# Kernel optimization log

Hardware: AMD Instinct MI355X
Metric: run time of the kernel (lower is better)

Reference implementation:

```python
import jax, jax.numpy as jnp
import numpy as np
from jax import lax

B, L = 8, 128
V, P = 30000, 50
EMB, POS = 300, 30
H = 256            # rnn_hidden per direction
H2 = 2 * H         # BiLSTM output dim
NBIO, NLAB = 9, 10
ROUNDS = 2
IN = EMB + POS
NEG = -100000000000.0


def setup_inputs() -> dict:
    key = jax.random.key(0)
    ks = jax.random.split(key, 25)
    tokens = jax.random.randint(ks[0], (B, L), 1, V)
    pos = jax.random.randint(ks[1], (B, L), 1, P)
    lens = jax.random.randint(ks[2], (B,), L // 2, L + 1)
    mask_s = (jnp.arange(L)[None, :] < lens[:, None]).astype(jnp.float32)

    def g(k, shape, s=0.05):
        return jax.random.normal(k, shape, dtype=jnp.float32) * s

    return dict(
        tokens=tokens, pos=pos, mask_s=mask_s,
        emb=g(ks[3], (V, EMB), 0.5), pos_emb=g(ks[4], (P, POS), 0.5),
        Wih_f=g(ks[5], (4 * H, IN)), Whh_f=g(ks[6], (4 * H, H)), b_f=g(ks[7], (4 * H,)),
        Wih_b=g(ks[8], (4 * H, IN)), Whh_b=g(ks[9], (4 * H, H)), b_b=g(ks[10], (4 * H,)),
        Wg_ih=g(ks[11], (3 * H2, NBIO)), Wg_hh=g(ks[12], (3 * H2, H2)),
        bg_ih=g(ks[13], (3 * H2,)), bg_hh=g(ks[14], (3 * H2,)),
        Wr_ih=g(ks[15], (3 * H2, NLAB)), Wr_hh=g(ks[16], (3 * H2, H2)),
        br_ih=g(ks[17], (3 * H2,)), br_hh=g(ks[18], (3 * H2,)),
        W_Lr=g(ks[19], (H2, 2 * H2)), b_Lr=g(ks[20], (H2,)),
        W_Cr=g(ks[21], (NLAB, H2)), b_Cr=g(ks[22], (NLAB,)),
        W_Cg=g(ks[23], (NBIO, H2)), b_Cg=g(ks[24], (NBIO,)),
    )


def lstm_dir(x, m, Wih, Whh, b, reverse):
    # x: [B,L,IN], m: [B,L]. Masked updates emulate pack_padded_sequence
    # (state held at padded steps; padded outputs zeroed by caller).
    Bn = x.shape[0]
    h0 = jnp.zeros((Bn, H), x.dtype)
    c0 = jnp.zeros((Bn, H), x.dtype)

    def step(carry, inp):
        h, c = carry
        xt, mt = inp  # [B,IN], [B,1]
        gates = xt @ Wih.T + h @ Whh.T + b
        i, f, g, o = jnp.split(gates, 4, axis=-1)
        i = jax.nn.sigmoid(i); f = jax.nn.sigmoid(f)
        g = jnp.tanh(g); o = jax.nn.sigmoid(o)
        c_new = f * c + i * g
        h_new = o * jnp.tanh(c_new)
        h = mt * h_new + (1.0 - mt) * h
        c = mt * c_new + (1.0 - mt) * c
        return (h, c), h

    xs = (jnp.swapaxes(x, 0, 1), m.T[:, :, None])
    _, hs = lax.scan(step, (h0, c0), xs, reverse=reverse)
    return jnp.swapaxes(hs, 0, 1)  # [B,L,H]


def gru_cell(x, h, Wih, Whh, bih, bhh):
    gi = x @ Wih.T + bih
    gh = h @ Whh.T + bhh
    ir, iz, inn = jnp.split(gi, 3, axis=-1)
    hr, hz, hn = jnp.split(gh, 3, axis=-1)
    r = jax.nn.sigmoid(ir + hr)
    z = jax.nn.sigmoid(iz + hz)
    n = jnp.tanh(inn + r * hn)
    return (1.0 - z) * n + z * h


def pair_scores(Hr, W_Lr, b_Lr, W_Cr, b_Cr):
    # Lr([e1;e2]) split: e12 @ W_Lr.T = e1 @ W1.T + e2 @ W2.T (avoids 4H concat)
    W1, W2 = W_Lr[:, :H2], W_Lr[:, H2:]
    a = jnp.einsum('blh,oh->blo', Hr, W1)  # [B,L,H2]
    b2 = jnp.einsum('blh,oh->blo', Hr, W2)
    e = jax.nn.relu(a[:, :, None, :] + b2[:, None, :, :] + b_Lr)  # [B,L,L,H2]
    return jax.nn.sigmoid(jnp.einsum('bsth,kh->bstk', e, W_Cr) + b_Cr)  # [B,L,L,NLAB]


def reference(tokens, pos, mask_s, emb, pos_emb,
              Wih_f, Whh_f, b_f, Wih_b, Whh_b, b_b,
              Wg_ih, Wg_hh, bg_ih, bg_hh,
              Wr_ih, Wr_hh, br_ih, br_hh,
              W_Lr, b_Lr, W_Cr, b_Cr, W_Cg, b_Cg):
    x = jnp.concatenate([emb[tokens], pos_emb[pos]], axis=2)  # [B,L,IN]
    hf = lstm_dir(x, mask_s, Wih_f, Whh_f, b_f, reverse=False)
    hb = lstm_dir(x, mask_s, Wih_b, Whh_b, b_b, reverse=True)
    Henc = jnp.concatenate([hf, hb], axis=2) * mask_s[:, :, None]  # [B,L,H2]

    m2 = mask_s[:, :, None] * mask_s[:, None, :]  # [B,L,L] pair mask
    m3 = m2[:, :, :, None]                        # [B,L,L,1]

    Hc, Hg, Hr = Henc, Henc, Henc
    for _ in range(ROUNDS):
        prob_Cg = jax.nn.softmax(Hg @ W_Cg.T + b_Cg, axis=2)        # [B,L,NBIO]
        prob_Cr = pair_scores(Hr, W_Lr, b_Lr, W_Cr, b_Cr)            # [B,L,L,NLAB]
        prob_Cr = jnp.where(m3 > 0, prob_Cr, NEG)
        prob_Cr = prob_Cr.max(axis=2)                                # [B,L,NLAB]
        hflat = Hc.reshape(-1, H2)
        Hg = gru_cell(prob_Cg.reshape(-1, NBIO), hflat, Wg_ih, Wg_hh, bg_ih, bg_hh).reshape(Hc.shape)
        Hr = gru_cell(prob_Cr.reshape(-1, NLAB), hflat, Wr_ih, Wr_hh, br_ih, br_hh).reshape(Hc.shape)
        Hc = Hc + Hr + Hg

    logits_Cg = jax.nn.log_softmax(Hg @ W_Cg.T + b_Cg, axis=2) * mask_s[:, :, None]
    logits_Cr = pair_scores(Hr, W_Lr, b_Lr, W_Cr, b_Cr) * m3
    return logits_Cg, logits_Cr
```

## Files before the change

### kernel.cpp

```cpp
#include <hip/hip_runtime.h>
#include <hip/hip_bf16.h>
#include <stdint.h>

#define DEVI __device__ __forceinline__

static constexpr int Bn = 8, Ln = 128;
static constexpr int EMBc = 300, POSc = 30, INc = 330;
static constexpr int KPAD = 384;
static constexpr int Hc = 256, H2c = 512, G4 = 1024, G3 = 1536;
static constexpr int G2 = 2048;
static constexpr int GHW = 3072;
static constexpr int NBIOc = 9, NLABc = 10;
static constexpr float NEGc = -100000000000.0f;

typedef __attribute__((ext_vector_type(8))) short bf16x8;
typedef __attribute__((ext_vector_type(4))) float f32x4;

DEVI float sigf(float x) { return 1.0f / (1.0f + __expf(-x)); }

DEVI unsigned short b16rne(float f) {
    union { float f; unsigned u; } v; v.f = f;
    unsigned u = v.u;
    return (unsigned short)((u + 0x7FFFu + ((u >> 16) & 1u)) >> 16);
}

__global__ void k_prep0(const int* __restrict__ tok, const int* __restrict__ pos,
                        const float* __restrict__ emb, const float* __restrict__ pemb,
                        const float* __restrict__ WihF, const float* __restrict__ WihB,
                        const float* __restrict__ bF, const float* __restrict__ bB,
                        ushort* __restrict__ x, ushort* __restrict__ WihFB,
                        float* __restrict__ biasFB) {
    int i = blockIdx.x * 256 + threadIdx.x;
    const int N0 = Bn * Ln * KPAD;
    const int N1 = N0 + G2 * KPAD;
    if (i < N0) {
        int bl = i / KPAD, c = i - bl * KPAD;
        float v = 0.f;
        if (c < EMBc) v = emb[tok[bl] * EMBc + c];
        else if (c < INc) v = pemb[pos[bl] * POSc + (c - EMBc)];
        x[i] = b16rne(v);
    } else if (i < N1) {
        int w = i - N0;
        int r = w / KPAD, c = w - r * KPAD;
        float v = 0.f;
        if (c < INc) v = (r < G4) ? WihF[(size_t)r * INc + c] : WihB[(size_t)(r - G4) * INc + c];
        WihFB[w] = b16rne(v);
    } else if (i < N1 + G2) {
        int j = i - N1;
        biasFB[j] = (j < G4) ? bF[j] : bB[j - G4];
    }
}

DEVI void gemm_tile(const ushort* __restrict__ A, const ushort* __restrict__ B,
                    const float* __restrict__ bias, float* __restrict__ C,
                    int N, int K, int m0, int n0,
                    ushort (*As)[72], ushort (*Bs)[72]) {
    int tid = threadIdx.x;
    int lane = tid & 63, wv = tid >> 6;
    int mw = (wv >> 1) * 32, nw = (wv & 1) * 32;
    int lr16 = lane & 15, g4 = lane >> 4;
    f32x4 acc[2][2] = {};
    for (int k0 = 0; k0 < K; k0 += 64) {
#pragma unroll
        for (int it = 0; it < 2; it++) {
            int idx = tid + it * 256;
            int r = idx >> 3, ch = idx & 7;
            uint4 av = *(const uint4*)(A + (size_t)(m0 + r) * K + k0 + ch * 8);
            *(uint4*)(&As[r][ch * 8]) = av;
            uint4 bv2 = *(const uint4*)(B + (size_t)(n0 + r) * K + k0 + ch * 8);
            *(uint4*)(&Bs[r][ch * 8]) = bv2;
        }
        __syncthreads();
#pragma unroll
        for (int ks = 0; ks < 2; ks++) {
            bf16x8 af[2], bfr[2];
#pragma unroll
            for (int i = 0; i < 2; i++) {
                af[i]  = *(const bf16x8*)(&As[mw + i * 16 + lr16][ks * 32 + g4 * 8]);
                bfr[i] = *(const bf16x8*)(&Bs[nw + i * 16 + lr16][ks * 32 + g4 * 8]);
            }
#pragma unroll
            for (int i = 0; i < 2; i++)
#pragma unroll
                for (int j = 0; j < 2; j++)
                    acc[i][j] = __builtin_amdgcn_mfma_f32_16x16x32_bf16(af[i], bfr[j], acc[i][j], 0, 0, 0);
        }
        __syncthreads();
    }
#pragma unroll
    for (int i = 0; i < 2; i++)
#pragma unroll
        for (int j = 0; j < 2; j++)
#pragma unroll
            for (int r2 = 0; r2 < 4; r2++) {
                int mm = m0 + mw + i * 16 + g4 * 4 + r2;
                int nn = n0 + nw + j * 16 + lr16;
                C[(size_t)mm * N + nn] = acc[i][j][r2] + (bias ? bias[nn] : 0.f);
            }
}

__global__ __launch_bounds__(256) void k_xproj(
    const ushort* __restrict__ x_bf, const ushort* __restrict__ WihFB,
    const float* __restrict__ biasFB, float* __restrict__ Xpre,
    const float* __restrict__ Wg_hh, const float* __restrict__ Wr_hh,
    const float* __restrict__ W_Lr, const float* __restrict__ bg_hh,
    const float* __restrict__ br_hh,
    ushort* __restrict__ WhhGR, ushort* __restrict__ WLrAB, float* __restrict__ biasGR) {
    int bid = blockIdx.x;
    __shared__ __align__(16) ushort As[64][72];
    __shared__ __align__(16) ushort Bs[64][72];
    if (bid < 512) {
        int nt = bid & 31, mt = bid >> 5;
        gemm_tile(x_bf, WihFB, biasFB, Xpre, G2, KPAD, mt * 64, nt * 64, As, Bs);
        return;
    }
    const int stride = 128 * 256;
    int pid = (bid - 512) * 256 + threadIdx.x;
    for (int idx = pid; idx < GHW * H2c; idx += stride) {
        int r = idx >> 9, c = idx & 511;
        float v = (r < G3) ? Wg_hh[(size_t)r * H2c + c] : Wr_hh[(size_t)(r - G3) * H2c + c];
        WhhGR[idx] = b16rne(v);
    }
    for (int idx = pid; idx < G4 * H2c; idx += stride) {
        int r = idx >> 9, c = idx & 511;
        float v = (r < H2c) ? W_Lr[(size_t)r * (2 * H2c) + c]
                            : W_Lr[(size_t)(r - H2c) * (2 * H2c) + H2c + c];
        WLrAB[idx] = b16rne(v);
    }
    for (int idx = pid; idx < GHW; idx += stride)
        biasGR[idx] = (idx < G3) ? bg_hh[idx] : br_hh[idx - G3];
}

__global__ __launch_bounds__(512) void k_lstm_mfma(
    const float* __restrict__ Xpre, const float* __restrict__ WhhF,
    const float* __restrict__ WhhB, const float* __restrict__ mask,
    float* __restrict__ Henc, ushort* __restrict__ HencB,
    unsigned long long* __restrict__ hG) {
    const int blk = blockIdx.x;
    const int d = blk >> 2, q = blk & 3;
    const float* Whh = d ? WhhB : WhhF;
    const int tid = threadIdx.x;
    const int lane = tid & 63, wv = tid >> 6;
    const int lr16 = lane & 15, g4 = lane >> 4;

    __shared__ __align__(16) uint32_t hlds[2][8 * 136];
    __shared__ float Glds[256][9];

    bf16x8 aw[16];
#pragma unroll
    for (int jt2 = 0; jt2 < 2; jt2++) {
        int jt = wv * 2 + jt2;
        int lr = jt * 16 + lr16;
        int g = lr >> 6, jj = lr & 63;
        int R = g * 256 + q * 64 + jj;
        const float* wr = Whh + (size_t)R * 256;
#pragma unroll
        for (int kt = 0; kt < 8; kt++) {
            int k0 = kt * 32 + g4 * 8;
            float4 f0 = *(const float4*)(wr + k0);
            float4 f1 = *(const float4*)(wr + k0 + 4);
            bf16x8 a;
            a[0] = (short)b16rne(f0.x); a[1] = (short)b16rne(f0.y);
            a[2] = (short)b16rne(f0.z); a[3] = (short)b16rne(f0.w);
            a[4] = (short)b16rne(f1.x); a[5] = (short)b16rne(f1.y);
            a[6] = (short)b16rne(f1.z); a[7] = (short)b16rne(f1.w);
            aw[jt2 * 8 + kt] = a;
        }
    }

    const int jj_t = tid & 63, b_t = tid >> 6;
    float hval = 0.f, cval = 0.f;
    const int bcol = lane & 15;
    const int bb = lane & 7;
    const int u1 = tid + 512;

    for (int s = 0; s < Ln; s++) {
        const int t = d ? (Ln - 1 - s) : s;

        const float* xrow = Xpre + ((size_t)(b_t * Ln + t)) * G2 + d * G4 + q * 64 + jj_t;
        float xg0 = xrow[0], xg1 = xrow[256], xg2 = xrow[512], xg3 = xrow[768];
        float mval = mask[b_t * Ln + t];

        const unsigned long long* slot = hG + ((size_t)(s & 1) * 2 + d) * 1024;
        unsigned long long ea, eb;
        do {
            ea = __hip_atomic_load(slot + tid, __ATOMIC_RELAXED, __HIP_MEMORY_SCOPE_AGENT);
            eb = __hip_atomic_load(slot + u1,  __ATOMIC_RELAXED, __HIP_MEMORY_SCOPE_AGENT);
        } while ((unsigned)(ea >> 32) != (unsigned)s || (unsigned)(eb >> 32) != (unsigned)s);
        uint32_t* hb = hlds[s & 1];
        hb[(tid >> 7) * 136 + (tid & 127)] = (uint32_t)ea;
        hb[(u1 >> 7) * 136 + (u1 & 127)]  = (uint32_t)eb;
        __syncthreads();

        bf16x8 bv[8];
#pragma unroll
        for (int kt = 0; kt < 8; kt++)
            bv[kt] = *(const bf16x8*)(&hb[bb * 136 + kt * 16 + g4 * 4]);

        f32x4 acc0 = {0.f, 0.f, 0.f, 0.f}, acc1 = {0.f, 0.f, 0.f, 0.f};
#pragma unroll
        for (int kt = 0; kt < 8; kt++) {
            acc0 = __builtin_amdgcn_mfma_f32_16x16x32_bf16(aw[kt], bv[kt], acc0, 0, 0, 0);
            acc1 = __builtin_amdgcn_mfma_f32_16x16x32_bf16(aw[8 + kt], bv[kt], acc1, 0, 0, 0);
        }

        if (bcol < 8) {
            int lrb0 = (wv * 2 + 0) * 16 + g4 * 4;
            int lrb1 = (wv * 2 + 1) * 16 + g4 * 4;
#pragma unroll
            for (int r2 = 0; r2 < 4; r2++) Glds[lrb0 + r2][bcol] = acc0[r2];
#pragma unroll
            for (int r2 = 0; r2 < 4; r2++) Glds[lrb1 + r2][bcol] = acc1[r2];
        }
        __syncthreads();

        float iv = sigf(xg0 + Glds[jj_t][b_t]);
        float fv = sigf(xg1 + Glds[64 + jj_t][b_t]);
        float gv = tanhf(xg2 + Glds[128 + jj_t][b_t]);
        float ov = sigf(xg3 + Glds[192 + jj_t][b_t]);
        float cn = fv * cval + iv * gv;
        float hn = ov * tanhf(cn);
        float hv = mval * hn + (1.f - mval) * hval;
        cval = mval * cn + (1.f - mval) * cval;
        hval = hv;

        int hbits = (int)b16rne(hv);
        int pbits = __shfl_xor(hbits, 1);
        if ((jj_t & 1) == 0) {
            uint32_t dataw = ((uint32_t)hbits & 0xFFFFu) | ((uint32_t)pbits << 16);
            unsigned long long word = ((unsigned long long)(unsigned)(s + 1) << 32) | dataw;
            __hip_atomic_store(hG + ((size_t)((s + 1) & 1) * 2 + d) * 1024 +
                                   b_t * 128 + q * 32 + (jj_t >> 1),
                               word, __ATOMIC_RELAXED, __HIP_MEMORY_SCOPE_AGENT);
        }
        float ho = hv * mval;
        size_t hidx = ((size_t)(b_t * Ln + t)) * H2c + d * Hc + q * 64 + jj_t;
        Henc[hidx] = ho;
        HencB[hidx] = b16rne(ho);
        __syncthreads();
    }
}

__global__ __launch_bounds__(256) void k_mega(
    int nGh,
    const ushort* __restrict__ Agh, const ushort* __restrict__ Bgh,
    const float* __restrict__ biasGh, float* __restrict__ Cgh,
    const ushort* __restrict__ Apc, const ushort* __restrict__ Bpc,
    float* __restrict__ Cpc,
    const float* __restrict__ Hp9, const float* __restrict__ W9,
    const float* __restrict__ b9, float* __restrict__ out9) {
    int bid = blockIdx.x;
    __shared__ __align__(16) ushort As[64][72];
    __shared__ __align__(16) ushort Bs[64][72];
    if (bid < nGh) {
        int nt = bid % 48, mt = bid / 48;
        gemm_tile(Agh, Bgh, biasGh, Cgh, GHW, H2c, mt * 64, nt * 64, As, Bs);
    } else if (bid < nGh + 256) {
        int b2 = bid - nGh;
        int nt = b2 & 15, mt = b2 >> 4;
        gemm_tile(Apc, Bpc, nullptr, Cpc, G4, H2c, mt * 64, nt * 64, As, Bs);
    } else {
        int b3 = bid - nGh - 256;
        int lane = threadIdx.x & 63, wvv = threadIdx.x >> 6;
        int row = b3 * 4 + wvv;
        const float4* h4 = (const float4*)(Hp9 + (size_t)row * H2c + lane * 8);
        float4 h0 = h4[0], h1 = h4[1];
        float acc[NBIOc];
#pragma unroll
        for (int k = 0; k < NBIOc; k++) {
            const float4* w4 = (const float4*)(W9 + (size_t)k * H2c + lane * 8);
            float4 w0 = w4[0], w1 = w4[1];
            acc[k] = h0.x * w0.x + h0.y * w0.y + h0.z * w0.z + h0.w * w0.w +
                     h1.x * w1.x + h1.y * w1.y + h1.z * w1.z + h1.w * w1.w;
        }
#pragma unroll
        for (int off = 32; off >= 1; off >>= 1)
#pragma unroll
            for (int k = 0; k < NBIOc; k++) acc[k] += __shfl_down(acc[k], off);
        if (lane == 0) {
#pragma unroll
            for (int k = 0; k < NBIOc; k++) out9[(size_t)row * NBIOc + k] = acc[k] + b9[k];
        }
    }
}

__global__ __launch_bounds__(128) void k_pairgru(
    const float* __restrict__ Cp, const float* __restrict__ bL,
    const float* __restrict__ WCr, const float* __restrict__ bCr,
    const float* __restrict__ mask, const float* __restrict__ cg,
    const float* __restrict__ gh,
    const float* __restrict__ Wg_ih, const float* __restrict__ bg_ih,
    const float* __restrict__ Wr_ih, const float* __restrict__ br_ih,
    const float* __restrict__ hprev,
    float* __restrict__ Hg_out, float* __restrict__ Hcb_out,
    ushort* __restrict__ Hrb_out, ushort* __restrict__ Hcbb_out) {
    int m = blockIdx.x;
    int b = m >> 7;
    __shared__ __align__(16) float As[H2c];
    __shared__ __align__(16) float Ws[NLABc][H2c];
    __shared__ float red[NLABc][128];
    __shared__ float pCr_s[NLABc];
    int tid = threadIdx.x;
    for (int i = tid; i < H2c; i += 128) As[i] = Cp[(size_t)m * G4 + i] + bL[i];
    for (int i = tid; i < NLABc * H2c; i += 128) Ws[i / H2c][i % H2c] = WCr[i];
    __syncthreads();
    {
        int t = tid;
        float m3 = mask[m] * mask[b * Ln + t];
        float outv[NLABc];
        if (m3 > 0.f) {
            float4 acc[NLABc];
#pragma unroll
            for (int k = 0; k < NLABc; k++) acc[k] = make_float4(0.f, 0.f, 0.f, 0.f);
            const float4* B4 = (const float4*)(Cp + (size_t)(b * Ln + t) * G4 + H2c);
            const float4* A4 = (const float4*)As;
            for (int qq = 0; qq < H2c / 4; qq++) {
                float4 a = A4[qq], bb = B4[qq];
                float4 e;
                e.x = fmaxf(a.x + bb.x, 0.f);
                e.y = fmaxf(a.y + bb.y, 0.f);
                e.z = fmaxf(a.z + bb.z, 0.f);
                e.w = fmaxf(a.w + bb.w, 0.f);
#pragma unroll
                for (int k = 0; k < NLABc; k++) {
                    float4 w = *(const float4*)(&Ws[k][qq * 4]);
                    acc[k].x += e.x * w.x; acc[k].y += e.y * w.y;
                    acc[k].z += e.z * w.z; acc[k].w += e.w * w.w;
                }
            }
#pragma unroll
            for (int k = 0; k < NLABc; k++)
                outv[k] = sigf(acc[k].x + acc[k].y + acc[k].z + acc[k].w + bCr[k]);
        } else {
#pragma unroll
            for (int k = 0; k < NLABc; k++) outv[k] = NEGc;
        }
#pragma unroll
        for (int k = 0; k < NLABc; k++) red[k][tid] = outv[k];
    }
    __syncthreads();
    for (int off = 64; off >= 1; off >>= 1) {
        if (tid < off) {
#pragma unroll
            for (int k = 0; k < NLABc; k++) red[k][tid] = fmaxf(red[k][tid], red[k][tid + off]);
        }
        __syncthreads();
    }
    if (tid < NLABc) pCr_s[tid] = red[tid][0];
    __syncthreads();

    float v[NBIOc], mx = -3.4e38f;
#pragma unroll
    for (int k = 0; k < NBIOc; k++) { v[k] = cg[m * NBIOc + k]; mx = fmaxf(mx, v[k]); }
    float ssum = 0.f;
#pragma unroll
    for (int k = 0; k < NBIOc; k++) { v[k] = __expf(v[k] - mx); ssum += v[k]; }
    float inv = 1.f / ssum;
#pragma unroll
    for (int k = 0; k < NBIOc; k++) v[k] *= inv;

    const float* g1b = gh + (size_t)m * GHW;
#pragma unroll
    for (int u = 0; u < 4; u++) {
        int j = tid + u * 128;
        size_t i = (size_t)m * H2c + j;

        float gr = bg_ih[j], gz = bg_ih[H2c + j], gn = bg_ih[2 * H2c + j];
#pragma unroll
        for (int k = 0; k < NBIOc; k++) {
            float pv = v[k];
            gr += Wg_ih[(size_t)j * NBIOc + k] * pv;
            gz += Wg_ih[(size_t)(H2c + j) * NBIOc + k] * pv;
            gn += Wg_ih[(size_t)(2 * H2c + j) * NBIOc + k] * pv;
        }
        float hp = hprev[i];
        float r1 = sigf(gr + g1b[j]);
        float z1 = sigf(gz + g1b[H2c + j]);
        float n1 = tanhf(gn + r1 * g1b[2 * H2c + j]);
        float hg = (1.f - z1) * n1 + z1 * hp;

        float rr = br_ih[j], rz = br_ih[H2c + j], rn = br_ih[2 * H2c + j];
#pragma unroll
        for (int k = 0; k < NLABc; k++) {
            float pv = pCr_s[k];
            rr += Wr_ih[(size_t)j * NLABc + k] * pv;
            rz += Wr_ih[(size_t)(H2c + j) * NLABc + k] * pv;
            rn += Wr_ih[(size_t)(2 * H2c + j) * NLABc + k] * pv;
        }
        const float* g2b = g1b + G3;
        float r2 = sigf(rr + g2b[j]);
        float z2 = sigf(rz + g2b[H2c + j]);
        float n2 = tanhf(rn + r2 * g2b[2 * H2c + j]);
        float hr = (1.f - z2) * n2 + z2 * hp;

        float hc = hp + hr + hg;
        Hg_out[i] = hg;
        Hcb_out[i] = hc;
        Hrb_out[i] = b16rne(hr);
        Hcbb_out[i] = b16rne(hc);
    }
}

__global__ __launch_bounds__(128) void k_final_out(
    const float* __restrict__ Cp, const float* __restrict__ bL,
    const float* __restrict__ WCr, const float* __restrict__ bCr,
    const float* __restrict__ mask, const float* __restrict__ cg,
    float* __restrict__ outp) {
    int bid = blockIdx.x;
    int tid = threadIdx.x;
    if (bid >= Bn * Ln) {
        int r = (bid - Bn * Ln) * 128 + tid;
        float v[NBIOc], mx = -3.4e38f;
#pragma unroll
        for (int k = 0; k < NBIOc; k++) { v[k] = cg[r * NBIOc + k]; mx = fmaxf(mx, v[k]); }
        float s = 0.f;
#pragma unroll
        for (int k = 0; k < NBIOc; k++) s += __expf(v[k] - mx);
        float lse = mx + __logf(s);
        float m = mask[r];
#pragma unroll
        for (int k = 0; k < NBIOc; k++) outp[r * NBIOc + k] = (v[k] - lse) * m;
        return;
    }
    int bs = bid;
    int b = bs >> 7;
    __shared__ __align__(16) float As[H2c];
    __shared__ __align__(16) float Ws[NLABc][H2c];
    for (int i = tid; i < H2c; i += 128) As[i] = Cp[(size_t)bs * G4 + i] + bL[i];
    for (int i = tid; i < NLABc * H2c; i += 128) Ws[i / H2c][i % H2c] = WCr[i];
    __syncthreads();
    int t = tid;
    float m3 = mask[bs] * mask[b * Ln + t];
    float outv[NLABc];
    if (m3 > 0.f) {
        float4 acc[NLABc];
#pragma unroll
        for (int k = 0; k < NLABc; k++) acc[k] = make_float4(0.f, 0.f, 0.f, 0.f);
        const float4* B4 = (const float4*)(Cp + (size_t)(b * Ln + t) * G4 + H2c);
        const float4* A4 = (const float4*)As;
        for (int qq = 0; qq < H2c / 4; qq++) {
            float4 a = A4[qq], bb = B4[qq];
            float4 e;
            e.x = fmaxf(a.x + bb.x, 0.f);
            e.y = fmaxf(a.y + bb.y, 0.f);
            e.z = fmaxf(a.z + bb.z, 0.f);
            e.w = fmaxf(a.w + bb.w, 0.f);
#pragma unroll
            for (int k = 0; k < NLABc; k++) {
                float4 w = *(const float4*)(&Ws[k][qq * 4]);
                acc[k].x += e.x * w.x; acc[k].y += e.y * w.y;
                acc[k].z += e.z * w.z; acc[k].w += e.w * w.w;
            }
        }
#pragma unroll
        for (int k = 0; k < NLABc; k++)
            outv[k] = sigf(acc[k].x + acc[k].y + acc[k].z + acc[k].w + bCr[k]);
    } else {
#pragma unroll
        for (int k = 0; k < NLABc; k++) outv[k] = 0.f;
    }
    size_t base = (size_t)(Bn * Ln * NBIOc) + ((size_t)bs * Ln + t) * NLABc;
#pragma unroll
    for (int k = 0; k < NLABc; k++) outp[base + k] = outv[k];
}

extern "C" void kernel_launch(void* const* d_in, const int* in_sizes, int n_in,
                              void* d_out, int out_size, void* d_ws, size_t ws_size,
                              hipStream_t stream) {
    const int*   tok   = (const int*)d_in[0];
    const int*   pos   = (const int*)d_in[1];
    const float* mask  = (const float*)d_in[2];
    const float* emb   = (const float*)d_in[3];
    const float* pemb  = (const float*)d_in[4];
    const float* WihF  = (const float*)d_in[5];
    const float* WhhF  = (const float*)d_in[6];
    const float* bF    = (const float*)d_in[7];
    const float* WihB  = (const float*)d_in[8];
    const float* WhhB  = (const float*)d_in[9];
    const float* bB    = (const float*)d_in[10];
    const float* Wg_ih = (const float*)d_in[11];
    const float* Wg_hh = (const float*)d_in[12];
    const float* bg_ih = (const float*)d_in[13];
    const float* bg_hh = (const float*)d_in[14];
    const float* Wr_ih = (const float*)d_in[15];
    const float* Wr_hh = (const float*)d_in[16];
    const float* br_ih = (const float*)d_in[17];
    const float* br_hh = (const float*)d_in[18];
    const float* W_Lr  = (const float*)d_in[19];
    const float* b_Lr  = (const float*)d_in[20];
    const float* W_Cr  = (const float*)d_in[21];
    const float* b_Cr  = (const float*)d_in[22];
    const float* W_Cg  = (const float*)d_in[23];
    const float* b_Cg  = (const float*)d_in[24];

    float* outp = (float*)d_out;
    float* ws = (float*)d_ws;

    unsigned long long* hG = (unsigned long long*)ws;
    size_t off = 8192;
    auto alloc = [&](size_t n) { off = (off + 3) & ~(size_t)3; float* p = ws + off; off += n; return p; };
    auto allocU = [&](size_t n_us) { off = (off + 3) & ~(size_t)3; ushort* p = (ushort*)(ws + off); off += (n_us + 1) / 2; return p; };

    float* R1 = alloc((size_t)G4 * GHW);
    float* Xpre = R1;
    float* gh   = R1;
    ushort* WihFB_bf = (ushort*)(R1 + (size_t)G4 * G2);
    ushort* x_bf     = (ushort*)(R1 + (size_t)G4 * G2 + 393216);
    float*  biasFB   = R1 + (size_t)G4 * G2 + 393216 + 196608;

    float*  pairC    = alloc((size_t)G4 * G4);
    ushort* WhhGR_bf = allocU((size_t)GHW * H2c);
    ushort* WLrAB_bf = allocU((size_t)G4 * H2c);
    float*  biasGR   = alloc(GHW);
    float*  Henc     = alloc((size_t)Bn * Ln * H2c);
    ushort* Henc_bf  = allocU((size_t)Bn * Ln * H2c);
    float*  Hg       = alloc((size_t)Bn * Ln * H2c);
    float*  Hcb      = alloc((size_t)Bn * Ln * H2c);
    ushort* Hr_bf    = allocU((size_t)Bn * Ln * H2c);
    ushort* Hcb_bf   = allocU((size_t)Bn * Ln * H2c);
    float*  cg       = alloc((size_t)Bn * Ln * NBIOc);
    (void)ws_size; (void)in_sizes; (void)n_in; (void)out_size;

    hipMemsetAsync(hG, 0, 8192 * sizeof(float), stream);

    {
        int total = Bn * Ln * KPAD + G2 * KPAD + G2;
        k_prep0<<<(total + 255) / 256, 256, 0, stream>>>(
            tok, pos, emb, pemb, WihF, WihB, bF, bB, x_bf, WihFB_bf, biasFB);
    }

    k_xproj<<<640, 256, 0, stream>>>(x_bf, WihFB_bf, biasFB, Xpre,
                                     Wg_hh, Wr_hh, W_Lr, bg_hh, br_hh,
                                     WhhGR_bf, WLrAB_bf, biasGR);

    k_lstm_mfma<<<8, 512, 0, stream>>>(Xpre, WhhF, WhhB, mask, Henc, Henc_bf, hG);

    const float*  Hgs    = Henc;
    const ushort* Hrs_bf = Henc_bf;
    const float*  Hcs    = Henc;
    const ushort* Hcs_bf = Henc_bf;
    for (int r = 0; r < 2; r++) {
        k_mega<<<768 + 512, 256, 0, stream>>>(768,
            Hcs_bf, WhhGR_bf, biasGR, gh,
            Hrs_bf, WLrAB_bf, pairC,
            Hgs, W_Cg, b_Cg, cg);
        k_pairgru<<<Bn * Ln, 128, 0, stream>>>(
            pairC, b_Lr, W_Cr, b_Cr, mask, cg, gh,
            Wg_ih, bg_ih, Wr_ih, br_ih, Hcs,
            Hg, Hcb, Hr_bf, Hcb_bf);
        Hgs = Hg; Hrs_bf = Hr_bf; Hcs = Hcb; Hcs_bf = Hcb_bf;
    }

    k_mega<<<512, 256, 0, stream>>>(0,
        nullptr, nullptr, nullptr, nullptr,
        Hrs_bf, WLrAB_bf, pairC,
        Hgs, W_Cg, b_Cg, cg);
    k_final_out<<<Bn * Ln + 8, 128, 0, stream>>>(pairC, b_Lr, W_Cr, b_Cr, mask, cg, outp);
}
```

Baseline: 432.5 us.

## Fold hG memset into prep kernel, transpose GRU input weights, move LSTM barrier

The hG flag buffer is now zeroed inside k_prep0 instead of by a separate hipMemsetAsync, which removes one launch. The small GRU input-weight matrices are transposed once in k_xproj so k_pairgru reads them coalesced across j rather than with a stride of 9 or 10. In the LSTM loop the barrier is moved before the Henc stores, so those global writes can overlap with the next step's work. These are three small, unrelated tweaks, and their combined effect on total time is likely minor.

Measured after the change: 432.9 us. About the same (+0.1%).

```diff
diff --git a/kernel.cpp b/kernel.cpp
--- a/kernel.cpp
+++ b/kernel.cpp
@@ -29,10 +29,12 @@
                         const float* __restrict__ WihF, const float* __restrict__ WihB,
                         const float* __restrict__ bF, const float* __restrict__ bB,
                         ushort* __restrict__ x, ushort* __restrict__ WihFB,
-                        float* __restrict__ biasFB) {
+                        float* __restrict__ biasFB, uint32_t* __restrict__ hG32) {
     int i = blockIdx.x * 256 + threadIdx.x;
     const int N0 = Bn * Ln * KPAD;
     const int N1 = N0 + G2 * KPAD;
+    const int N2 = N1 + G2;
+    const int N3 = N2 + 8192;
     if (i < N0) {
         int bl = i / KPAD, c = i - bl * KPAD;
         float v = 0.f;
@@ -45,9 +47,11 @@
         float v = 0.f;
         if (c < INc) v = (r < G4) ? WihF[(size_t)r * INc + c] : WihB[(size_t)(r - G4) * INc + c];
         WihFB[w] = b16rne(v);
-    } else if (i < N1 + G2) {
+    } else if (i < N2) {
         int j = i - N1;
         biasFB[j] = (j < G4) ? bF[j] : bB[j - G4];
+    } else if (i < N3) {
+        __hip_atomic_store(&hG32[i - N2], 0u, __ATOMIC_RELAXED, __HIP_MEMORY_SCOPE_AGENT);
     }
 }
 
@@ -105,7 +109,9 @@
     const float* __restrict__ Wg_hh, const float* __restrict__ Wr_hh,
     const float* __restrict__ W_Lr, const float* __restrict__ bg_hh,
     const float* __restrict__ br_hh,
-    ushort* __restrict__ WhhGR, ushort* __restrict__ WLrAB, float* __restrict__ biasGR) {
+    const float* __restrict__ Wg_ih, const float* __restrict__ Wr_ih,
+    ushort* __restrict__ WhhGR, ushort* __restrict__ WLrAB, float* __restrict__ biasGR,
+    float* __restrict__ WgihT, float* __restrict__ WrihT) {
     int bid = blockIdx.x;
     __shared__ __align__(16) ushort As[64][72];
     __shared__ __align__(16) ushort Bs[64][72];
@@ -129,6 +135,14 @@
     }
     for (int idx = pid; idx < GHW; idx += stride)
         biasGR[idx] = (idx < G3) ? bg_hh[idx] : br_hh[idx - G3];
+    for (int idx = pid; idx < NBIOc * G3; idx += stride) {
+        int k = idx / G3, rj = idx - k * G3;
+        WgihT[idx] = Wg_ih[(size_t)rj * NBIOc + k];
+    }
+    for (int idx = pid; idx < NLABc * G3; idx += stride) {
+        int k = idx / G3, rj = idx - k * G3;
+        WrihT[idx] = Wr_ih[(size_t)rj * NLABc + k];
+    }
 }
 
 __global__ __launch_bounds__(512) void k_lstm_mfma(
@@ -233,11 +247,12 @@
                                    b_t * 128 + q * 32 + (jj_t >> 1),
                                word, __ATOMIC_RELAXED, __HIP_MEMORY_SCOPE_AGENT);
         }
+        __syncthreads();
+
         float ho = hv * mval;
         size_t hidx = ((size_t)(b_t * Ln + t)) * H2c + d * Hc + q * 64 + jj_t;
         Henc[hidx] = ho;
         HencB[hidx] = b16rne(ho);
-        __syncthreads();
     }
 }
 
@@ -289,8 +304,8 @@
     const float* __restrict__ WCr, const float* __restrict__ bCr,
     const float* __restrict__ mask, const float* __restrict__ cg,
     const float* __restrict__ gh,
-    const float* __restrict__ Wg_ih, const float* __restrict__ bg_ih,
-    const float* __restrict__ Wr_ih, const float* __restrict__ br_ih,
+    const float* __restrict__ WgihT, const float* __restrict__ bg_ih,
+    const float* __restrict__ WrihT, const float* __restrict__ br_ih,
     const float* __restrict__ hprev,
     float* __restrict__ Hg_out, float* __restrict__ Hcb_out,
     ushort* __restrict__ Hrb_out, ushort* __restrict__ Hcbb_out) {
@@ -369,9 +384,9 @@
 #pragma unroll
         for (int k = 0; k < NBIOc; k++) {
             float pv = v[k];
-            gr += Wg_ih[(size_t)j * NBIOc + k] * pv;
-            gz += Wg_ih[(size_t)(H2c + j) * NBIOc + k] * pv;
-            gn += Wg_ih[(size_t)(2 * H2c + j) * NBIOc + k] * pv;
+            gr += WgihT[k * G3 + j] * pv;
+            gz += WgihT[k * G3 + H2c + j] * pv;
+            gn += WgihT[k * G3 + 2 * H2c + j] * pv;
         }
         float hp = hprev[i];
         float r1 = sigf(gr + g1b[j]);
@@ -383,9 +398,9 @@
 #pragma unroll
         for (int k = 0; k < NLABc; k++) {
             float pv = pCr_s[k];
-            rr += Wr_ih[(size_t)j * NLABc + k] * pv;
-            rz += Wr_ih[(size_t)(H2c + j) * NLABc + k] * pv;
-            rn += Wr_ih[(size_t)(2 * H2c + j) * NLABc + k] * pv;
+            rr += WrihT[k * G3 + j] * pv;
+            rz += WrihT[k * G3 + H2c + j] * pv;
+            rn += WrihT[k * G3 + 2 * H2c + j] * pv;
         }
         const float* g2b = g1b + G3;
         float r2 = sigf(rr + g2b[j]);
@@ -512,6 +527,8 @@
     ushort* WhhGR_bf = allocU((size_t)GHW * H2c);
     ushort* WLrAB_bf = allocU((size_t)G4 * H2c);
     float*  biasGR   = alloc(GHW);
+    float*  WgihT    = alloc((size_t)NBIOc * G3);
+    float*  WrihT    = alloc((size_t)NLABc * G3);
     float*  Henc     = alloc((size_t)Bn * Ln * H2c);
     ushort* Henc_bf  = allocU((size_t)Bn * Ln * H2c);
     float*  Hg       = alloc((size_t)Bn * Ln * H2c);
@@ -521,17 +538,17 @@
     float*  cg       = alloc((size_t)Bn * Ln * NBIOc);
     (void)ws_size; (void)in_sizes; (void)n_in; (void)out_size;
 
-    hipMemsetAsync(hG, 0, 8192 * sizeof(float), stream);
-
     {
-        int total = Bn * Ln * KPAD + G2 * KPAD + G2;
+        int total = Bn * Ln * KPAD + G2 * KPAD + G2 + 8192;
         k_prep0<<<(total + 255) / 256, 256, 0, stream>>>(
-            tok, pos, emb, pemb, WihF, WihB, bF, bB, x_bf, WihFB_bf, biasFB);
+            tok, pos, emb, pemb, WihF, WihB, bF, bB, x_bf, WihFB_bf, biasFB,
+            (uint32_t*)hG);
     }
 
     k_xproj<<<640, 256, 0, stream>>>(x_bf, WihFB_bf, biasFB, Xpre,
                                      Wg_hh, Wr_hh, W_Lr, bg_hh, br_hh,
-                                     WhhGR_bf, WLrAB_bf, biasGR);
+                                     Wg_ih, Wr_ih,
+                                     WhhGR_bf, WLrAB_bf, biasGR, WgihT, WrihT);
 
     k_lstm_mfma<<<8, 512, 0, stream>>>(Xpre, WhhF, WhhB, mask, Henc, Henc_bf, hG);
 
@@ -546,7 +563,7 @@
             Hgs, W_Cg, b_Cg, cg);
         k_pairgru<<<Bn * Ln, 128, 0, stream>>>(
             pairC, b_Lr, W_Cr, b_Cr, mask, cg, gh,
-            Wg_ih, bg_ih, Wr_ih, br_ih, Hcs,
+            WgihT, bg_ih, WrihT, br_ih, Hcs,
             Hg, Hcb, Hr_bf, Hcb_bf);
         Hgs = Hg; Hrs_bf = Hr_bf; Hcs = Hcb; Hcs_bf = Hcb_bf;
     }
```
